# Kernel tuning notes

Measured on AMD Instinct MI355X. Metric: run time of the kernel, lower is better.

Reference implementation:

```python
import jax, jax.numpy as jnp
import numpy as np

N = 50000   # nodes
E = 200000  # edges
G = 2048    # graphs in batch
H = 300     # hidden_dim
L = 5       # nlayer
AF, AV = 9, 128   # atom features, vocab per feature
BF, BV = 3, 16    # bond features, vocab per feature


def setup_inputs() -> dict:
    key = jax.random.key(0)
    ks = jax.random.split(key, 10)
    s = 0.05
    batch = jnp.sort(jax.random.randint(ks[0], (N,), 0, G))
    x = jax.random.randint(ks[1], (N, AF), 0, AV)
    edge_index = jax.random.randint(ks[2], (2, E), 0, N)
    edge_attr = jax.random.randint(ks[3], (E, BF), 0, BV)
    atom_emb = jax.random.normal(ks[4], (AF * AV, H), dtype=jnp.float32) * s
    bond_emb = jax.random.normal(ks[5], (BF * BV, H), dtype=jnp.float32) * s
    W1 = jax.random.normal(ks[6], (L, H, 2 * H), dtype=jnp.float32) * s
    b1 = jnp.zeros((L, 2 * H), jnp.float32)
    g1 = jnp.ones((L, 2 * H), jnp.float32)
    be1 = jnp.zeros((L, 2 * H), jnp.float32)
    W2 = jax.random.normal(ks[7], (L, 2 * H, H), dtype=jnp.float32) * s
    b2 = jnp.zeros((L, H), jnp.float32)
    g2 = jnp.ones((L, H), jnp.float32)   # outer BatchNorm gamma
    be2 = jnp.zeros((L, H), jnp.float32)  # outer BatchNorm beta
    return dict(batch=batch, x=x, edge_index=edge_index, edge_attr=edge_attr,
                atom_emb=atom_emb, bond_emb=bond_emb,
                W1=W1, b1=b1, g1=g1, be1=be1, W2=W2, b2=b2, g2=g2, be2=be2)


def _bn(z, g, b):
    # training-mode BatchNorm1d over the node/batch dim
    m = z.mean(0)
    v = z.var(0)
    return (z - m) * jax.lax.rsqrt(v + 1e-5) * g + b


def reference(batch, x, edge_index, edge_attr, atom_emb, bond_emb,
              W1, b1, g1, be1, W2, b2, g2, be2):
    # AtomEncoder / BondEncoder: sum of per-feature embeddings (flat-table gather)
    h = atom_emb[x + jnp.arange(AF) * AV].sum(axis=1)          # [N, H]
    e = bond_emb[edge_attr + jnp.arange(BF) * BV].sum(axis=1)  # [E, H]
    src, dst = edge_index[0], edge_index[1]
    for i in range(L):
        # GINEConv: out = MLP((1+eps)*x + sum_j relu(x_j + e_ij)), eps=0
        msg = jax.nn.relu(h[src] + e)                          # [E, H]
        agg = jax.ops.segment_sum(msg, dst, num_segments=N)    # [N, H]
        z = h + agg
        z = jax.nn.relu(_bn(z @ W1[i] + b1[i], g1[i], be1[i])) # Linear+BN+ReLU
        z = z @ W2[i] + b2[i]                                  # Linear
        z = _bn(z, g2[i], be2[i])                              # outer BatchNorm
        h = z if i == L - 1 else jax.nn.relu(z)                # dropout p=0.0 -> identity
    xpool = jax.ops.segment_sum(h, batch, num_segments=G)     # global_add_pool
    return (h, xpool)
```

## Files before the change

### kernel.cpp

```cpp
#include <hip/hip_runtime.h>

#define N_NODES 50000
#define N_EDGES 200000
#define N_GRAPHS 2048
#define HDIM 300
#define HDIM2 600
#define NLAYER 5
#define K1P 320
#define N1P 640
#define N2P 384

#define MT1 ((N_NODES + 127) / 128)
#define NWG1 (5 * MT1)
#define NWG2 (3 * MT1)

#define SCAN_BLK 1024
#define NSCAN ((N_NODES + SCAN_BLK - 1) / SCAN_BLK)

typedef __attribute__((ext_vector_type(8))) _Float16 f16x8;
typedef __attribute__((ext_vector_type(8))) unsigned short ushort8;
typedef __attribute__((ext_vector_type(4))) float f32x4;

__device__ __forceinline__ unsigned short f2h(float f) {
    _Float16 h = (_Float16)f;
    return __builtin_bit_cast(unsigned short, h);
}
__device__ __forceinline__ float h2f(unsigned short u) {
    _Float16 h = __builtin_bit_cast(_Float16, u);
    return (float)h;
}

__device__ __forceinline__ int lower_bound_i(const int* a, int n, int key) {
    int lo = 0, hi = n;
    while (lo < hi) { int mid = (lo + hi) >> 1; if (a[mid] < key) lo = mid + 1; else hi = mid; }
    return lo;
}

__device__ __forceinline__ int xcd_swz(int orig, int nwg) {
    int q = nwg >> 3, r = nwg & 7;
    int xcd = orig & 7;
    int base = (xcd < r) ? xcd * (q + 1) : r * (q + 1) + (xcd - r) * q;
    return base + (orig >> 3);
}

__global__ void k_init(int* deg, int* fill, float* s1, float* q1, float* s2, float* q2) {
    int i = blockIdx.x * blockDim.x + threadIdx.x;
    if (i < N_NODES) { deg[i] = 0; fill[i] = 0; }
    if (i < N1P)     { s1[i] = 0.f; q1[i] = 0.f; }
    if (i < K1P)     { s2[i] = 0.f; q2[i] = 0.f; }
}

__global__ void k_atom(const int* __restrict__ x, const float* __restrict__ atom_emb,
                       unsigned short* __restrict__ hf) {
    int idx = blockIdx.x * blockDim.x + threadIdx.x;
    if (idx >= N_NODES * K1P) return;
    int n = idx / K1P;
    int c = idx - n * K1P;
    if (c >= HDIM) { hf[idx] = 0; return; }
    const int* xr = x + n * 9;
    float acc = 0.f;
#pragma unroll
    for (int f = 0; f < 9; ++f) {
        int row = xr[f] + f * 128;
        acc += atom_emb[(size_t)row * HDIM + c];
    }
    hf[idx] = f2h(acc);
}

__global__ void k_deg(const int* __restrict__ dst, int* deg) {
    int j = blockIdx.x * blockDim.x + threadIdx.x;
    if (j < N_EDGES) atomicAdd(&deg[dst[j]], 1);
}

__global__ void k_scan1(const int* __restrict__ deg, int* __restrict__ part,
                        int* __restrict__ psum) {
    __shared__ int buf[SCAN_BLK];
    int b = blockIdx.x, tid = threadIdx.x;
    int i = b * SCAN_BLK + tid;
    int v = (i < N_NODES) ? deg[i] : 0;
    buf[tid] = v;
    __syncthreads();
    for (int off = 1; off < SCAN_BLK; off <<= 1) {
        int t = (tid >= off) ? buf[tid - off] : 0;
        __syncthreads();
        buf[tid] += t;
        __syncthreads();
    }
    if (i < N_NODES) part[i] = buf[tid];
    if (tid == SCAN_BLK - 1) psum[b] = buf[tid];
}

__global__ void k_scan2(int* __restrict__ psum) {
    __shared__ int buf[64];
    int tid = threadIdx.x;
    int v = (tid < NSCAN) ? psum[tid] : 0;
    buf[tid] = v;
    __syncthreads();
    for (int off = 1; off < 64; off <<= 1) {
        int t = (tid >= off) ? buf[tid - off] : 0;
        __syncthreads();
        buf[tid] += t;
        __syncthreads();
    }
    if (tid < NSCAN) psum[tid] = buf[tid] - v;
}

__global__ void k_scan3(const int* __restrict__ part, const int* __restrict__ psum,
                        int* __restrict__ rowptr) {
    int i = blockIdx.x * blockDim.x + threadIdx.x;
    if (i == 0) rowptr[0] = 0;
    if (i < N_NODES) rowptr[i + 1] = part[i] + psum[i / SCAN_BLK];
}

__global__ void k_fill(const int* __restrict__ src, const int* __restrict__ dst,
                       const int* __restrict__ eattr, const int* __restrict__ rowptr,
                       int* fill, int* __restrict__ csr_src, int* __restrict__ csr_att) {
    int j = blockIdx.x * blockDim.x + threadIdx.x;
    if (j < N_EDGES) {
        int d = dst[j];
        int p = atomicAdd(&fill[d], 1);
        int pos = rowptr[d] + p;
        csr_src[pos] = src[j];
        csr_att[pos] = eattr[j * 3 + 0] | (eattr[j * 3 + 1] << 8) | (eattr[j * 3 + 2] << 16);
    }
}

__global__ void k_wconv(const float* __restrict__ W, unsigned short* __restrict__ Bt,
                        int K, int NC, int KPAD, int NPAD) {
    int idx = blockIdx.x * blockDim.x + threadIdx.x;
    int tot = NLAYER * NPAD * KPAD;
    if (idx >= tot) return;
    int l = idx / (NPAD * KPAD);
    int rem = idx - l * NPAD * KPAD;
    int n = rem / KPAD;
    int k = rem - n * KPAD;
    float v = (k < K && n < NC) ? W[((size_t)l * K + k) * NC + n] : 0.f;
    Bt[idx] = f2h(v);
}

template <bool BN>
__global__ __launch_bounds__(128) void k_msg(const unsigned short* __restrict__ hsrc,
                                             const float* __restrict__ sc,
                                             const float* __restrict__ sh,
                                             const int* __restrict__ rowptr,
                                             const int* __restrict__ csr_src,
                                             const int* __restrict__ csr_att,
                                             const float* __restrict__ bond_emb,
                                             unsigned short* __restrict__ zin) {
    int n = blockIdx.x;
    int t = threadIdx.x;
    int cols[3] = { t, t + 128, t + 256 };
    float scv[3] = {0.f, 0.f, 0.f}, shv[3] = {0.f, 0.f, 0.f};
    float acc[3] = {0.f, 0.f, 0.f};
#pragma unroll
    for (int q = 0; q < 3; ++q) {
        int c = cols[q];
        if (c < HDIM) {
            if (BN) { scv[q] = sc[c]; shv[q] = sh[c]; }
            float v = h2f(hsrc[(size_t)n * K1P + c]);
            if (BN) v = fmaxf(v * scv[q] + shv[q], 0.f);
            acc[q] = v;
        }
    }

    int beg = rowptr[n], end = rowptr[n + 1];
    int p = beg;
    for (; p + 2 <= end; p += 2) {
        int s0 = csr_src[p],     a0 = csr_att[p];
        int s1 = csr_src[p + 1], a1 = csr_att[p + 1];
        const unsigned short* h0 = hsrc + (size_t)s0 * K1P;
        const unsigned short* h1 = hsrc + (size_t)s1 * K1P;
        const float* e00 = bond_emb + (size_t)(a0 & 0xff) * HDIM;
        const float* e01 = bond_emb + (size_t)(16 + ((a0 >> 8) & 0xff)) * HDIM;
        const float* e02 = bond_emb + (size_t)(32 + ((a0 >> 16) & 0xff)) * HDIM;
        const float* e10 = bond_emb + (size_t)(a1 & 0xff) * HDIM;
        const float* e11 = bond_emb + (size_t)(16 + ((a1 >> 8) & 0xff)) * HDIM;
        const float* e12 = bond_emb + (size_t)(32 + ((a1 >> 16) & 0xff)) * HDIM;
#pragma unroll
        for (int q = 0; q < 3; ++q) {
            int c = cols[q];
            if (c < HDIM) {
                float v0 = h2f(h0[c]);
                float v1 = h2f(h1[c]);
                if (BN) {
                    v0 = fmaxf(v0 * scv[q] + shv[q], 0.f);
                    v1 = fmaxf(v1 * scv[q] + shv[q], 0.f);
                }
                float m0 = v0 + e00[c] + e01[c] + e02[c];
                float m1 = v1 + e10[c] + e11[c] + e12[c];
                acc[q] += fmaxf(m0, 0.f) + fmaxf(m1, 0.f);
            }
        }
    }
    if (p < end) {
        int s0 = csr_src[p], a0 = csr_att[p];
        const unsigned short* h0 = hsrc + (size_t)s0 * K1P;
        const float* e00 = bond_emb + (size_t)(a0 & 0xff) * HDIM;
        const float* e01 = bond_emb + (size_t)(16 + ((a0 >> 8) & 0xff)) * HDIM;
        const float* e02 = bond_emb + (size_t)(32 + ((a0 >> 16) & 0xff)) * HDIM;
#pragma unroll
        for (int q = 0; q < 3; ++q) {
            int c = cols[q];
            if (c < HDIM) {
                float v0 = h2f(h0[c]);
                if (BN) v0 = fmaxf(v0 * scv[q] + shv[q], 0.f);
                float m0 = v0 + e00[c] + e01[c] + e02[c];
                acc[q] += fmaxf(m0, 0.f);
            }
        }
    }
    unsigned short* zr = zin + (size_t)n * K1P;
#pragma unroll
    for (int q = 0; q < 3; ++q) {
        int c = cols[q];
        if (c < HDIM) zr[c] = f2h(acc[q]);
        else if (c < K1P) zr[c] = 0;
    }
}

__global__ __launch_bounds__(256) void k_mfma1(const unsigned short* __restrict__ A,
                                               const unsigned short* __restrict__ Bt,
                                               const float* __restrict__ bias,
                                               unsigned short* __restrict__ Ch,
                                               float* __restrict__ gsum,
                                               float* __restrict__ gssq) {
    __shared__ unsigned short tA[2][128 * 32];
    __shared__ unsigned short tB[2][128 * 32];
    __shared__ float csum[128], cssq[128];

    const int tid = threadIdx.x;
    const int lane = tid & 63, wid = tid >> 6;
    const int wm = wid >> 1, wn = wid & 1;
    const int wgid = xcd_swz(blockIdx.x, NWG1);
    const int n0 = (wgid % 5) * 128, m0 = (wgid / 5) * 128;
    const int fr = lane & 15, fq = lane >> 4;

    f32x4 acc[4][4] = {};
    const int arow = lane >> 2;
    const int achk = (lane & 3) * 8;
    constexpr int NT = K1P / 32;

    auto stage = [&](int buf, int kt) {
        const int k0 = kt * 32;
#pragma unroll
        for (int i = 0; i < 2; ++i) {
            int grp = i * 4 + wid;
            int grow = m0 + grp * 16 + arow;
            if (grow >= N_NODES) grow = N_NODES - 1;
            const unsigned short* ga = A + (size_t)grow * K1P + k0 + achk;
            __builtin_amdgcn_global_load_lds((const __attribute__((address_space(1))) void*)ga,
                                             (__attribute__((address_space(3))) void*)&tA[buf][grp * 512],
                                             16, 0, 0);
            int gn = n0 + grp * 16 + arow;
            const unsigned short* gb = Bt + (size_t)gn * K1P + k0 + achk;
            __builtin_amdgcn_global_load_lds((const __attribute__((address_space(1))) void*)gb,
                                             (__attribute__((address_space(3))) void*)&tB[buf][grp * 512],
                                             16, 0, 0);
        }
    };

    stage(0, 0);
    __syncthreads();

    int cur = 0;
    for (int kt = 0; kt < NT; ++kt) {
        if (kt + 1 < NT) stage(cur ^ 1, kt + 1);

        f16x8 af[4], bfr[4];
#pragma unroll
        for (int t = 0; t < 4; ++t) {
            af[t]  = *(const f16x8*)&tA[cur][(wm * 64 + t * 16 + fr) * 32 + fq * 8];
            bfr[t] = *(const f16x8*)&tB[cur][(wn * 64 + t * 16 + fr) * 32 + fq * 8];
        }
#pragma unroll
        for (int mt = 0; mt < 4; ++mt)
#pragma unroll
            for (int nt = 0; nt < 4; ++nt)
                acc[mt][nt] = __builtin_amdgcn_mfma_f32_16x16x32_f16(af[mt], bfr[nt], acc[mt][nt], 0, 0, 0);

        __syncthreads();
        cur ^= 1;
    }

    float bv[4];
#pragma unroll
    for (int nt = 0; nt < 4; ++nt) {
        int col = n0 + wn * 64 + nt * 16 + fr;
        bv[nt] = (col < HDIM2) ? bias[col] : 0.f;
    }
    if (tid < 128) { csum[tid] = 0.f; cssq[tid] = 0.f; }
    __syncthreads();

    float colS[4] = {0.f, 0.f, 0.f, 0.f};
    float colQ[4] = {0.f, 0.f, 0.f, 0.f};
#pragma unroll
    for (int mt = 0; mt < 4; ++mt) {
#pragma unroll
        for (int r = 0; r < 4; ++r) {
            int row = m0 + wm * 64 + mt * 16 + fq * 4 + r;
            bool rok = row < N_NODES;
#pragma unroll
            for (int nt = 0; nt < 4; ++nt) {
                int col = n0 + wn * 64 + nt * 16 + fr;
                float v = acc[mt][nt][r] + bv[nt];
                if (rok && col < HDIM2) {
                    Ch[(size_t)row * N1P + col] = f2h(v);
                    colS[nt] += v;
                    colQ[nt] += v * v;
                } else if (rok) {
                    Ch[(size_t)row * N1P + col] = 0;
                }
            }
        }
    }
#pragma unroll
    for (int nt = 0; nt < 4; ++nt) {
        int c = wn * 64 + nt * 16 + fr;
        atomicAdd(&csum[c], colS[nt]);
        atomicAdd(&cssq[c], colQ[nt]);
    }
    __syncthreads();
    if (tid < 128) {
        int col = n0 + tid;
        if (col < HDIM2) {
            atomicAdd(&gsum[col], csum[tid]);
            atomicAdd(&gssq[col], cssq[tid]);
        }
    }
}

__global__ __launch_bounds__(256) void k_mfma2(const unsigned short* __restrict__ z1,
                                               const unsigned short* __restrict__ Bt,
                                               const float* __restrict__ bias,
                                               const unsigned short* __restrict__ scaleAh,
                                               const unsigned short* __restrict__ shiftAh,
                                               unsigned short* __restrict__ Ch,
                                               float* __restrict__ gsum,
                                               float* __restrict__ gssq) {
    __shared__ unsigned short tA[2][128 * 32];
    __shared__ unsigned short tB[2][128 * 32];
    __shared__ float csum[128], cssq[128];

    const int tid = threadIdx.x;
    const int lane = tid & 63, wid = tid >> 6;
    const int wm = wid >> 1, wn = wid & 1;
    const int wgid = xcd_swz(blockIdx.x, NWG2);
    const int n0 = (wgid % 3) * 128, m0 = (wgid / 3) * 128;
    const int fr = lane & 15, fq = lane >> 4;

    f32x4 acc[4][4] = {};
    const int arow = lane >> 2;
    const int achk = (lane & 3) * 8;
    constexpr int NT = N1P / 32;

    auto stage = [&](int buf, int kt) {
        const int k0 = kt * 32;
#pragma unroll
        for (int i = 0; i < 2; ++i) {
            int grp = i * 4 + wid;
            int grow = m0 + grp * 16 + arow;
            if (grow >= N_NODES) grow = N_NODES - 1;
            const unsigned short* ga = z1 + (size_t)grow * N1P + k0 + achk;
            __builtin_amdgcn_global_load_lds((const __attribute__((address_space(1))) void*)ga,
                                             (__attribute__((address_space(3))) void*)&tA[buf][grp * 512],
                                             16, 0, 0);
            int gn = n0 + grp * 16 + arow;
            const unsigned short* gb = Bt + (size_t)gn * N1P + k0 + achk;
            __builtin_amdgcn_global_load_lds((const __attribute__((address_space(1))) void*)gb,
                                             (__attribute__((address_space(3))) void*)&tB[buf][grp * 512],
                                             16, 0, 0);
        }
    };

    stage(0, 0);
    __syncthreads();

    int cur = 0;
    for (int kt = 0; kt < NT; ++kt) {
        if (kt + 1 < NT) stage(cur ^ 1, kt + 1);

        const int kc = kt * 32 + fq * 8;
        f16x8 sa = *(const f16x8*)&scaleAh[kc];
        f16x8 sb = *(const f16x8*)&shiftAh[kc];
        f16x8 af[4], bfr[4];
#pragma unroll
        for (int t = 0; t < 4; ++t) {
            f16x8 z = *(const f16x8*)&tA[cur][(wm * 64 + t * 16 + fr) * 32 + fq * 8];
            f16x8 r;
#pragma unroll
            for (int j = 0; j < 8; ++j) {
                _Float16 v = z[j] * sa[j] + sb[j];
                r[j] = (v > (_Float16)0) ? v : (_Float16)0;
            }
            af[t] = r;
            bfr[t] = *(const f16x8*)&tB[cur][(wn * 64 + t * 16 + fr) * 32 + fq * 8];
        }
#pragma unroll
        for (int mt = 0; mt < 4; ++mt)
#pragma unroll
            for (int nt = 0; nt < 4; ++nt)
                acc[mt][nt] = __builtin_amdgcn_mfma_f32_16x16x32_f16(af[mt], bfr[nt], acc[mt][nt], 0, 0, 0);

        __syncthreads();
        cur ^= 1;
    }

    float bv[4];
#pragma unroll
    for (int nt = 0; nt < 4; ++nt) {
        int col = n0 + wn * 64 + nt * 16 + fr;
        bv[nt] = (col < HDIM) ? bias[col] : 0.f;
    }
    if (tid < 128) { csum[tid] = 0.f; cssq[tid] = 0.f; }
    __syncthreads();

    float colS[4] = {0.f, 0.f, 0.f, 0.f};
    float colQ[4] = {0.f, 0.f, 0.f, 0.f};
#pragma unroll
    for (int mt = 0; mt < 4; ++mt) {
#pragma unroll
        for (int r = 0; r < 4; ++r) {
            int row = m0 + wm * 64 + mt * 16 + fq * 4 + r;
            bool rok = row < N_NODES;
#pragma unroll
            for (int nt = 0; nt < 4; ++nt) {
                int col = n0 + wn * 64 + nt * 16 + fr;
                float v = acc[mt][nt][r] + bv[nt];
                if (rok && col < HDIM) {
                    Ch[(size_t)row * K1P + col] = f2h(v);
                    colS[nt] += v;
                    colQ[nt] += v * v;
                } else if (rok && col < K1P) {
                    Ch[(size_t)row * K1P + col] = 0;
                }
            }
        }
    }
#pragma unroll
    for (int nt = 0; nt < 4; ++nt) {
        int c = wn * 64 + nt * 16 + fr;
        atomicAdd(&csum[c], colS[nt]);
        atomicAdd(&cssq[c], colQ[nt]);
    }
    __syncthreads();
    if (tid < 128) {
        int col = n0 + tid;
        if (col < HDIM) {
            atomicAdd(&gsum[col], csum[tid]);
            atomicAdd(&gssq[col], cssq[tid]);
        }
    }
}

__global__ void k_fin(const float* __restrict__ gsum, const float* __restrict__ gssq,
                      const float* __restrict__ gamma, const float* __restrict__ beta,
                      int C, int CPAD, float* __restrict__ scale, float* __restrict__ shift,
                      unsigned short* scaleh, unsigned short* shifth,
                      float* zs, float* zq, int CZ) {
    int i = blockIdx.x * blockDim.x + threadIdx.x;
    if (i < CPAD) {
        float sc = 0.f, sh = 0.f;
        if (i < C) {
            float m = gsum[i] * (1.f / (float)N_NODES);
            float v = gssq[i] * (1.f / (float)N_NODES) - m * m;
            float rs = rsqrtf(v + 1e-5f);
            sc = rs * gamma[i];
            sh = beta[i] - m * sc;
        }
        scale[i] = sc;
        shift[i] = sh;
        if (scaleh) { scaleh[i] = f2h(sc); shifth[i] = f2h(sh); }
    }
    if (i < CZ) { zs[i] = 0.f; zq[i] = 0.f; }
}

__global__ void k_normf(const unsigned short* __restrict__ z2,
                        const float* __restrict__ scale, const float* __restrict__ shift,
                        float* __restrict__ out_h) {
    int idx = blockIdx.x * blockDim.x + threadIdx.x;
    if (idx >= N_NODES * (K1P / 4)) return;
    int row = idx / (K1P / 4);
    int c = (idx % (K1P / 4)) * 4;
    if (c >= HDIM) return;
    const unsigned short* zr = z2 + (size_t)row * K1P + c;
    float4 o;
    o.x = h2f(zr[0]) * scale[c + 0] + shift[c + 0];
    o.y = h2f(zr[1]) * scale[c + 1] + shift[c + 1];
    o.z = h2f(zr[2]) * scale[c + 2] + shift[c + 2];
    o.w = h2f(zr[3]) * scale[c + 3] + shift[c + 3];
    *(float4*)(out_h + (size_t)row * HDIM + c) = o;
}

__global__ __launch_bounds__(128) void k_pool(const float* __restrict__ hfin,
                                              const int* __restrict__ batch,
                                              float* __restrict__ xpool) {
    int g = blockIdx.x;
    int t = threadIdx.x;
    int start = lower_bound_i(batch, N_NODES, g);
    int end   = lower_bound_i(batch, N_NODES, g + 1);
    int cols[3] = { t, t + 128, t + 256 };
    float acc[3] = {0.f, 0.f, 0.f};
    for (int n = start; n < end; ++n) {
        const float* hr = hfin + (size_t)n * HDIM;
#pragma unroll
        for (int q = 0; q < 3; ++q)
            if (cols[q] < HDIM) acc[q] += hr[cols[q]];
    }
#pragma unroll
    for (int q = 0; q < 3; ++q)
        if (cols[q] < HDIM) xpool[(size_t)g * HDIM + cols[q]] = acc[q];
}

extern "C" void kernel_launch(void* const* d_in, const int* in_sizes, int n_in,
                              void* d_out, int out_size, void* d_ws, size_t ws_size,
                              hipStream_t stream) {
    const int*   batch    = (const int*)d_in[0];
    const int*   x        = (const int*)d_in[1];
    const int*   eidx     = (const int*)d_in[2];
    const int*   eattr    = (const int*)d_in[3];
    const float* atom_emb = (const float*)d_in[4];
    const float* bond_emb = (const float*)d_in[5];
    const float* W1 = (const float*)d_in[6];
    const float* b1 = (const float*)d_in[7];
    const float* g1 = (const float*)d_in[8];
    const float* be1 = (const float*)d_in[9];
    const float* W2 = (const float*)d_in[10];
    const float* b2 = (const float*)d_in[11];
    const float* g2 = (const float*)d_in[12];
    const float* be2 = (const float*)d_in[13];

    const int* src = eidx;
    const int* dst = eidx + N_EDGES;

    float* out_h    = (float*)d_out;
    float* out_pool = (float*)d_out + (size_t)N_NODES * HDIM;

    char* ws = (char*)d_ws;
    size_t off = 0;
    auto alloc = [&](size_t bytes) -> void* {
        void* p = ws + off;
        off += (bytes + 255) & ~(size_t)255;
        return p;
    };
    unsigned short* hf   = (unsigned short*)alloc((size_t)N_NODES * K1P * 2);
    unsigned short* zin  = (unsigned short*)alloc((size_t)N_NODES * K1P * 2);
    unsigned short* z1   = (unsigned short*)alloc((size_t)N_NODES * N1P * 2);
    unsigned short* z2   = (unsigned short*)alloc((size_t)N_NODES * K1P * 2);
    unsigned short* W1t  = (unsigned short*)alloc((size_t)NLAYER * N1P * K1P * 2);
    unsigned short* W2t  = (unsigned short*)alloc((size_t)NLAYER * N2P * N1P * 2);
    int* rowptr  = (int*)alloc((N_NODES + 1) * sizeof(int));
    int* deg     = (int*)alloc(N_NODES * sizeof(int));
    int* fill    = (int*)alloc(N_NODES * sizeof(int));
    int* part    = (int*)alloc(N_NODES * sizeof(int));
    int* psum    = (int*)alloc(64 * sizeof(int));
    int* csr_src = (int*)alloc(N_EDGES * sizeof(int));
    int* csr_att = (int*)alloc(N_EDGES * sizeof(int));
    float* s1     = (float*)alloc(N1P * sizeof(float));
    float* q1     = (float*)alloc(N1P * sizeof(float));
    float* scale1 = (float*)alloc(N1P * sizeof(float));
    float* shift1 = (float*)alloc(N1P * sizeof(float));
    unsigned short* scale1h = (unsigned short*)alloc(N1P * sizeof(short));
    unsigned short* shift1h = (unsigned short*)alloc(N1P * sizeof(short));
    float* s2     = (float*)alloc(K1P * sizeof(float));
    float* q2     = (float*)alloc(K1P * sizeof(float));
    float* scale2 = (float*)alloc(K1P * sizeof(float));
    float* shift2 = (float*)alloc(K1P * sizeof(float));

    k_init<<<(N_NODES + 255) / 256, 256, 0, stream>>>(deg, fill, s1, q1, s2, q2);
    k_atom<<<(N_NODES * K1P + 255) / 256, 256, 0, stream>>>(x, atom_emb, hf);
    k_deg<<<(N_EDGES + 255) / 256, 256, 0, stream>>>(dst, deg);
    k_scan1<<<NSCAN, SCAN_BLK, 0, stream>>>(deg, part, psum);
    k_scan2<<<1, 64, 0, stream>>>(psum);
    k_scan3<<<(N_NODES + 255) / 256, 256, 0, stream>>>(part, psum, rowptr);
    k_fill<<<(N_EDGES + 255) / 256, 256, 0, stream>>>(src, dst, eattr, rowptr,
                                                      fill, csr_src, csr_att);
    {
        int tot1 = NLAYER * N1P * K1P;
        k_wconv<<<(tot1 + 255) / 256, 256, 0, stream>>>(W1, W1t, HDIM, HDIM2, K1P, N1P);
        int tot2 = NLAYER * N2P * N1P;
        k_wconv<<<(tot2 + 255) / 256, 256, 0, stream>>>(W2, W2t, HDIM2, HDIM, N1P, N2P);
    }

    for (int l = 0; l < NLAYER; ++l) {
        if (l == 0) {
            k_msg<false><<<N_NODES, 128, 0, stream>>>(hf, nullptr, nullptr,
                                                      rowptr, csr_src, csr_att, bond_emb, zin);
        } else {
            k_msg<true><<<N_NODES, 128, 0, stream>>>(z2, scale2, shift2,
                                                     rowptr, csr_src, csr_att, bond_emb, zin);
        }

        k_mfma1<<<NWG1, 256, 0, stream>>>(
            zin, W1t + (size_t)l * N1P * K1P, b1 + (size_t)l * HDIM2, z1, s1, q1);

        k_fin<<<3, 256, 0, stream>>>(s1, q1, g1 + (size_t)l * HDIM2, be1 + (size_t)l * HDIM2,
                                     HDIM2, N1P, scale1, shift1, scale1h, shift1h,
                                     s2, q2, K1P);

        k_mfma2<<<NWG2, 256, 0, stream>>>(
            z1, W2t + (size_t)l * N2P * N1P, b2 + (size_t)l * HDIM,
            scale1h, shift1h, z2, s2, q2);

        k_fin<<<3, 256, 0, stream>>>(s2, q2, g2 + (size_t)l * HDIM, be2 + (size_t)l * HDIM,
                                     HDIM, K1P, scale2, shift2, nullptr, nullptr,
                                     s1, q1, N1P);
    }

    k_normf<<<(N_NODES * (K1P / 4) + 255) / 256, 256, 0, stream>>>(
        z2, scale2, shift2, out_h);

    k_pool<<<N_GRAPHS, 128, 0, stream>>>(out_h, batch, out_pool);
}
```

Before: 1.221 ms.

## Map one wavefront per node in message kernel and double GEMM K-step

The message-aggregation kernel now assigns one 64-lane wavefront per node (four nodes per 256-thread block) with five columns per lane, replacing one 128-thread block per node where many threads idled on the 300-wide row. Both MFMA GEMM kernels now stage 64-wide K tiles (two 32-wide halves) per pipeline step, halving the number of barriers and staging rounds. The larger tiles double the LDS footprint per block, which may reduce occupancy.

```diff
diff --git a/kernel.cpp b/kernel.cpp
--- a/kernel.cpp
+++ b/kernel.cpp
@@ -139,7 +139,7 @@
 }
 
 template <bool BN>
-__global__ __launch_bounds__(128) void k_msg(const unsigned short* __restrict__ hsrc,
+__global__ __launch_bounds__(256) void k_msg(const unsigned short* __restrict__ hsrc,
                                              const float* __restrict__ sc,
                                              const float* __restrict__ sh,
                                              const int* __restrict__ rowptr,
@@ -147,14 +147,15 @@
                                              const int* __restrict__ csr_att,
                                              const float* __restrict__ bond_emb,
                                              unsigned short* __restrict__ zin) {
-    int n = blockIdx.x;
-    int t = threadIdx.x;
-    int cols[3] = { t, t + 128, t + 256 };
-    float scv[3] = {0.f, 0.f, 0.f}, shv[3] = {0.f, 0.f, 0.f};
-    float acc[3] = {0.f, 0.f, 0.f};
-#pragma unroll
-    for (int q = 0; q < 3; ++q) {
-        int c = cols[q];
+    int wid = threadIdx.x >> 6, lane = threadIdx.x & 63;
+    int n = blockIdx.x * 4 + wid;
+    if (n >= N_NODES) return;
+
+    float scv[5], shv[5], acc[5];
+#pragma unroll
+    for (int q = 0; q < 5; ++q) {
+        int c = lane + 64 * q;
+        scv[q] = 0.f; shv[q] = 0.f; acc[q] = 0.f;
         if (c < HDIM) {
             if (BN) { scv[q] = sc[c]; shv[q] = sh[c]; }
             float v = h2f(hsrc[(size_t)n * K1P + c]);
@@ -177,8 +178,8 @@
         const float* e11 = bond_emb + (size_t)(16 + ((a1 >> 8) & 0xff)) * HDIM;
         const float* e12 = bond_emb + (size_t)(32 + ((a1 >> 16) & 0xff)) * HDIM;
 #pragma unroll
-        for (int q = 0; q < 3; ++q) {
-            int c = cols[q];
+        for (int q = 0; q < 5; ++q) {
+            int c = lane + 64 * q;
             if (c < HDIM) {
                 float v0 = h2f(h0[c]);
                 float v1 = h2f(h1[c]);
@@ -199,8 +200,8 @@
         const float* e01 = bond_emb + (size_t)(16 + ((a0 >> 8) & 0xff)) * HDIM;
         const float* e02 = bond_emb + (size_t)(32 + ((a0 >> 16) & 0xff)) * HDIM;
 #pragma unroll
-        for (int q = 0; q < 3; ++q) {
-            int c = cols[q];
+        for (int q = 0; q < 5; ++q) {
+            int c = lane + 64 * q;
             if (c < HDIM) {
                 float v0 = h2f(h0[c]);
                 if (BN) v0 = fmaxf(v0 * scv[q] + shv[q], 0.f);
@@ -211,10 +212,9 @@
     }
     unsigned short* zr = zin + (size_t)n * K1P;
 #pragma unroll
-    for (int q = 0; q < 3; ++q) {
-        int c = cols[q];
-        if (c < HDIM) zr[c] = f2h(acc[q]);
-        else if (c < K1P) zr[c] = 0;
+    for (int q = 0; q < 5; ++q) {
+        int c = lane + 64 * q;
+        zr[c] = (c < HDIM) ? f2h(acc[q]) : 0;
     }
 }
 
@@ -224,8 +224,8 @@
                                                unsigned short* __restrict__ Ch,
                                                float* __restrict__ gsum,
                                                float* __restrict__ gssq) {
-    __shared__ unsigned short tA[2][128 * 32];
-    __shared__ unsigned short tB[2][128 * 32];
+    __shared__ unsigned short tA[2][8192];
+    __shared__ unsigned short tB[2][8192];
     __shared__ float csum[128], cssq[128];
 
     const int tid = threadIdx.x;
@@ -238,24 +238,27 @@
     f32x4 acc[4][4] = {};
     const int arow = lane >> 2;
     const int achk = (lane & 3) * 8;
-    constexpr int NT = K1P / 32;
-
-    auto stage = [&](int buf, int kt) {
-        const int k0 = kt * 32;
-#pragma unroll
-        for (int i = 0; i < 2; ++i) {
-            int grp = i * 4 + wid;
-            int grow = m0 + grp * 16 + arow;
-            if (grow >= N_NODES) grow = N_NODES - 1;
-            const unsigned short* ga = A + (size_t)grow * K1P + k0 + achk;
-            __builtin_amdgcn_global_load_lds((const __attribute__((address_space(1))) void*)ga,
-                                             (__attribute__((address_space(3))) void*)&tA[buf][grp * 512],
-                                             16, 0, 0);
-            int gn = n0 + grp * 16 + arow;
-            const unsigned short* gb = Bt + (size_t)gn * K1P + k0 + achk;
-            __builtin_amdgcn_global_load_lds((const __attribute__((address_space(1))) void*)gb,
-                                             (__attribute__((address_space(3))) void*)&tB[buf][grp * 512],
-                                             16, 0, 0);
+    constexpr int NT2 = K1P / 64;
+
+    auto stage = [&](int buf, int kt2) {
+        const int k0 = kt2 * 64;
+#pragma unroll
+        for (int hh = 0; hh < 2; ++hh) {
+#pragma unroll
+            for (int i = 0; i < 2; ++i) {
+                int grp = i * 4 + wid;
+                int grow = m0 + grp * 16 + arow;
+                if (grow >= N_NODES) grow = N_NODES - 1;
+                const unsigned short* ga = A + (size_t)grow * K1P + k0 + hh * 32 + achk;
+                __builtin_amdgcn_global_load_lds((const __attribute__((address_space(1))) void*)ga,
+                                                 (__attribute__((address_space(3))) void*)&tA[buf][hh * 4096 + grp * 512],
+                                                 16, 0, 0);
+                int gn = n0 + grp * 16 + arow;
+                const unsigned short* gb = Bt + (size_t)gn * K1P + k0 + hh * 32 + achk;
+                __builtin_amdgcn_global_load_lds((const __attribute__((address_space(1))) void*)gb,
+                                                 (__attribute__((address_space(3))) void*)&tB[buf][hh * 4096 + grp * 512],
+                                                 16, 0, 0);
+            }
         }
     };
 
@@ -263,20 +266,23 @@
     __syncthreads();
 
     int cur = 0;
-    for (int kt = 0; kt < NT; ++kt) {
-        if (kt + 1 < NT) stage(cur ^ 1, kt + 1);
-
-        f16x8 af[4], bfr[4];
-#pragma unroll
-        for (int t = 0; t < 4; ++t) {
-            af[t]  = *(const f16x8*)&tA[cur][(wm * 64 + t * 16 + fr) * 32 + fq * 8];
-            bfr[t] = *(const f16x8*)&tB[cur][(wn * 64 + t * 16 + fr) * 32 + fq * 8];
-        }
-#pragma unroll
-        for (int mt = 0; mt < 4; ++mt)
-#pragma unroll
-            for (int nt = 0; nt < 4; ++nt)
-                acc[mt][nt] = __builtin_amdgcn_mfma_f32_16x16x32_f16(af[mt], bfr[nt], acc[mt][nt], 0, 0, 0);
+    for (int kt2 = 0; kt2 < NT2; ++kt2) {
+        if (kt2 + 1 < NT2) stage(cur ^ 1, kt2 + 1);
+
+#pragma unroll
+        for (int hh = 0; hh < 2; ++hh) {
+            f16x8 af[4], bfr[4];
+#pragma unroll
+            for (int t = 0; t < 4; ++t) {
+                af[t]  = *(const f16x8*)&tA[cur][hh * 4096 + (wm * 64 + t * 16 + fr) * 32 + fq * 8];
+                bfr[t] = *(const f16x8*)&tB[cur][hh * 4096 + (wn * 64 + t * 16 + fr) * 32 + fq * 8];
+            }
+#pragma unroll
+            for (int mt = 0; mt < 4; ++mt)
+#pragma unroll
+                for (int nt = 0; nt < 4; ++nt)
+                    acc[mt][nt] = __builtin_amdgcn_mfma_f32_16x16x32_f16(af[mt], bfr[nt], acc[mt][nt], 0, 0, 0);
+        }
 
         __syncthreads();
         cur ^= 1;
@@ -337,8 +343,8 @@
                                                unsigned short* __restrict__ Ch,
                                                float* __restrict__ gsum,
                                                float* __restrict__ gssq) {
-    __shared__ unsigned short tA[2][128 * 32];
-    __shared__ unsigned short tB[2][128 * 32];
+    __shared__ unsigned short tA[2][8192];
+    __shared__ unsigned short tB[2][8192];
     __shared__ float csum[128], cssq[128];
 
     const int tid = threadIdx.x;
@@ -351,24 +357,27 @@
     f32x4 acc[4][4] = {};
     const int arow = lane >> 2;
     const int achk = (lane & 3) * 8;
-    constexpr int NT = N1P / 32;
-
-    auto stage = [&](int buf, int kt) {
-        const int k0 = kt * 32;
-#pragma unroll
-        for (int i = 0; i < 2; ++i) {
-            int grp = i * 4 + wid;
-            int grow = m0 + grp * 16 + arow;
-            if (grow >= N_NODES) grow = N_NODES - 1;
-            const unsigned short* ga = z1 + (size_t)grow * N1P + k0 + achk;
-            __builtin_amdgcn_global_load_lds((const __attribute__((address_space(1))) void*)ga,
-                                             (__attribute__((address_space(3))) void*)&tA[buf][grp * 512],
-                                             16, 0, 0);
-            int gn = n0 + grp * 16 + arow;
-            const unsigned short* gb = Bt + (size_t)gn * N1P + k0 + achk;
-            __builtin_amdgcn_global_load_lds((const __attribute__((address_space(1))) void*)gb,
-                                             (__attribute__((address_space(3))) void*)&tB[buf][grp * 512],
-                                             16, 0, 0);
+    constexpr int NT2 = N1P / 64;
+
+    auto stage = [&](int buf, int kt2) {
+        const int k0 = kt2 * 64;
+#pragma unroll
+        for (int hh = 0; hh < 2; ++hh) {
+#pragma unroll
+            for (int i = 0; i < 2; ++i) {
+                int grp = i * 4 + wid;
+                int grow = m0 + grp * 16 + arow;
+                if (grow >= N_NODES) grow = N_NODES - 1;
+                const unsigned short* ga = z1 + (size_t)grow * N1P + k0 + hh * 32 + achk;
+                __builtin_amdgcn_global_load_lds((const __attribute__((address_space(1))) void*)ga,
+                                                 (__attribute__((address_space(3))) void*)&tA[buf][hh * 4096 + grp * 512],
+                                                 16, 0, 0);
+                int gn = n0 + grp * 16 + arow;
+                const unsigned short* gb = Bt + (size_t)gn * N1P + k0 + hh * 32 + achk;
+                __builtin_amdgcn_global_load_lds((const __attribute__((address_space(1))) void*)gb,
+                                                 (__attribute__((address_space(3))) void*)&tB[buf][hh * 4096 + grp * 512],
+                                                 16, 0, 0);
+            }
         }
     };
 
@@ -376,30 +385,33 @@
     __syncthreads();
 
     int cur = 0;
-    for (int kt = 0; kt < NT; ++kt) {
-        if (kt + 1 < NT) stage(cur ^ 1, kt + 1);
-
-        const int kc = kt * 32 + fq * 8;
-        f16x8 sa = *(const f16x8*)&scaleAh[kc];
-        f16x8 sb = *(const f16x8*)&shiftAh[kc];
-        f16x8 af[4], bfr[4];
-#pragma unroll
-        for (int t = 0; t < 4; ++t) {
-            f16x8 z = *(const f16x8*)&tA[cur][(wm * 64 + t * 16 + fr) * 32 + fq * 8];
-            f16x8 r;
-#pragma unroll
-            for (int j = 0; j < 8; ++j) {
-                _Float16 v = z[j] * sa[j] + sb[j];
-                r[j] = (v > (_Float16)0) ? v : (_Float16)0;
-            }
-            af[t] = r;
-            bfr[t] = *(const f16x8*)&tB[cur][(wn * 64 + t * 16 + fr) * 32 + fq * 8];
-        }
-#pragma unroll
-        for (int mt = 0; mt < 4; ++mt)
-#pragma unroll
-            for (int nt = 0; nt < 4; ++nt)
-                acc[mt][nt] = __builtin_amdgcn_mfma_f32_16x16x32_f16(af[mt], bfr[nt], acc[mt][nt], 0, 0, 0);
+    for (int kt2 = 0; kt2 < NT2; ++kt2) {
+        if (kt2 + 1 < NT2) stage(cur ^ 1, kt2 + 1);
+
+#pragma unroll
+        for (int hh = 0; hh < 2; ++hh) {
+            const int kc = kt2 * 64 + hh * 32 + fq * 8;
+            f16x8 sa = *(const f16x8*)&scaleAh[kc];
+            f16x8 sb = *(const f16x8*)&shiftAh[kc];
+            f16x8 af[4], bfr[4];
+#pragma unroll
+            for (int t = 0; t < 4; ++t) {
+                f16x8 z = *(const f16x8*)&tA[cur][hh * 4096 + (wm * 64 + t * 16 + fr) * 32 + fq * 8];
+                f16x8 r;
+#pragma unroll
+                for (int j = 0; j < 8; ++j) {
+                    _Float16 v = z[j] * sa[j] + sb[j];
+                    r[j] = (v > (_Float16)0) ? v : (_Float16)0;
+                }
+                af[t] = r;
+                bfr[t] = *(const f16x8*)&tB[cur][hh * 4096 + (wn * 64 + t * 16 + fr) * 32 + fq * 8];
+            }
+#pragma unroll
+            for (int mt = 0; mt < 4; ++mt)
+#pragma unroll
+                for (int nt = 0; nt < 4; ++nt)
+                    acc[mt][nt] = __builtin_amdgcn_mfma_f32_16x16x32_f16(af[mt], bfr[nt], acc[mt][nt], 0, 0, 0);
+        }
 
         __syncthreads();
         cur ^= 1;
@@ -581,13 +593,14 @@
         k_wconv<<<(tot2 + 255) / 256, 256, 0, stream>>>(W2, W2t, HDIM2, HDIM, N1P, N2P);
     }
 
+    int msg_grid = (N_NODES + 3) / 4;
     for (int l = 0; l < NLAYER; ++l) {
         if (l == 0) {
-            k_msg<false><<<N_NODES, 128, 0, stream>>>(hf, nullptr, nullptr,
+            k_msg<false><<<msg_grid, 256, 0, stream>>>(hf, nullptr, nullptr,
+                                                       rowptr, csr_src, csr_att, bond_emb, zin);
+        } else {
+            k_msg<true><<<msg_grid, 256, 0, stream>>>(z2, scale2, shift2,
                                                       rowptr, csr_src, csr_att, bond_emb, zin);
-        } else {
-            k_msg<true><<<N_NODES, 128, 0, stream>>>(z2, scale2, shift2,
-                                                     rowptr, csr_src, csr_att, bond_emb, zin);
         }
 
         k_mfma1<<<NWG1, 256, 0, stream>>>(
```

Result: slower. 1.308 ms (+7.2%).

## Map one wavefront per node in message kernel and add occupancy hints to GEMMs

Applied to the files above, without the earlier changes.

The message/aggregation kernel changes from one 128-thread block per node (3 columns per thread, with idle lanes in the last pass) to one 64-lane wavefront per node, four nodes per 256-thread block, each lane covering 5 columns. This cuts the block count by four and removes cross-wave work for a single node, which lowers launch and scheduling overhead and avoids partially idle waves. The two MFMA GEMM kernels also get min-blocks-per-CU launch bounds (4 and 3), which limit register use to raise occupancy but may cause spills.

```diff
diff --git a/kernel.cpp b/kernel.cpp
--- a/kernel.cpp
+++ b/kernel.cpp
@@ -139,7 +139,7 @@
 }
 
 template <bool BN>
-__global__ __launch_bounds__(128) void k_msg(const unsigned short* __restrict__ hsrc,
+__global__ __launch_bounds__(256) void k_msg(const unsigned short* __restrict__ hsrc,
                                              const float* __restrict__ sc,
                                              const float* __restrict__ sh,
                                              const int* __restrict__ rowptr,
@@ -147,14 +147,15 @@
                                              const int* __restrict__ csr_att,
                                              const float* __restrict__ bond_emb,
                                              unsigned short* __restrict__ zin) {
-    int n = blockIdx.x;
-    int t = threadIdx.x;
-    int cols[3] = { t, t + 128, t + 256 };
-    float scv[3] = {0.f, 0.f, 0.f}, shv[3] = {0.f, 0.f, 0.f};
-    float acc[3] = {0.f, 0.f, 0.f};
-#pragma unroll
-    for (int q = 0; q < 3; ++q) {
-        int c = cols[q];
+    int wid = threadIdx.x >> 6, lane = threadIdx.x & 63;
+    int n = blockIdx.x * 4 + wid;
+    if (n >= N_NODES) return;
+
+    float scv[5], shv[5], acc[5];
+#pragma unroll
+    for (int q = 0; q < 5; ++q) {
+        int c = lane + 64 * q;
+        scv[q] = 0.f; shv[q] = 0.f; acc[q] = 0.f;
         if (c < HDIM) {
             if (BN) { scv[q] = sc[c]; shv[q] = sh[c]; }
             float v = h2f(hsrc[(size_t)n * K1P + c]);
@@ -177,8 +178,8 @@
         const float* e11 = bond_emb + (size_t)(16 + ((a1 >> 8) & 0xff)) * HDIM;
         const float* e12 = bond_emb + (size_t)(32 + ((a1 >> 16) & 0xff)) * HDIM;
 #pragma unroll
-        for (int q = 0; q < 3; ++q) {
-            int c = cols[q];
+        for (int q = 0; q < 5; ++q) {
+            int c = lane + 64 * q;
             if (c < HDIM) {
                 float v0 = h2f(h0[c]);
                 float v1 = h2f(h1[c]);
@@ -199,8 +200,8 @@
         const float* e01 = bond_emb + (size_t)(16 + ((a0 >> 8) & 0xff)) * HDIM;
         const float* e02 = bond_emb + (size_t)(32 + ((a0 >> 16) & 0xff)) * HDIM;
 #pragma unroll
-        for (int q = 0; q < 3; ++q) {
-            int c = cols[q];
+        for (int q = 0; q < 5; ++q) {
+            int c = lane + 64 * q;
             if (c < HDIM) {
                 float v0 = h2f(h0[c]);
                 if (BN) v0 = fmaxf(v0 * scv[q] + shv[q], 0.f);
@@ -211,19 +212,18 @@
     }
     unsigned short* zr = zin + (size_t)n * K1P;
 #pragma unroll
-    for (int q = 0; q < 3; ++q) {
-        int c = cols[q];
-        if (c < HDIM) zr[c] = f2h(acc[q]);
-        else if (c < K1P) zr[c] = 0;
-    }
-}
-
-__global__ __launch_bounds__(256) void k_mfma1(const unsigned short* __restrict__ A,
-                                               const unsigned short* __restrict__ Bt,
-                                               const float* __restrict__ bias,
-                                               unsigned short* __restrict__ Ch,
-                                               float* __restrict__ gsum,
-                                               float* __restrict__ gssq) {
+    for (int q = 0; q < 5; ++q) {
+        int c = lane + 64 * q;
+        zr[c] = (c < HDIM) ? f2h(acc[q]) : 0;
+    }
+}
+
+__global__ __launch_bounds__(256, 4) void k_mfma1(const unsigned short* __restrict__ A,
+                                                  const unsigned short* __restrict__ Bt,
+                                                  const float* __restrict__ bias,
+                                                  unsigned short* __restrict__ Ch,
+                                                  float* __restrict__ gsum,
+                                                  float* __restrict__ gssq) {
     __shared__ unsigned short tA[2][128 * 32];
     __shared__ unsigned short tB[2][128 * 32];
     __shared__ float csum[128], cssq[128];
@@ -329,14 +329,14 @@
     }
 }
 
-__global__ __launch_bounds__(256) void k_mfma2(const unsigned short* __restrict__ z1,
-                                               const unsigned short* __restrict__ Bt,
-                                               const float* __restrict__ bias,
-                                               const unsigned short* __restrict__ scaleAh,
-                                               const unsigned short* __restrict__ shiftAh,
-                                               unsigned short* __restrict__ Ch,
-                                               float* __restrict__ gsum,
-                                               float* __restrict__ gssq) {
+__global__ __launch_bounds__(256, 3) void k_mfma2(const unsigned short* __restrict__ z1,
+                                                  const unsigned short* __restrict__ Bt,
+                                                  const float* __restrict__ bias,
+                                                  const unsigned short* __restrict__ scaleAh,
+                                                  const unsigned short* __restrict__ shiftAh,
+                                                  unsigned short* __restrict__ Ch,
+                                                  float* __restrict__ gsum,
+                                                  float* __restrict__ gssq) {
     __shared__ unsigned short tA[2][128 * 32];
     __shared__ unsigned short tB[2][128 * 32];
     __shared__ float csum[128], cssq[128];
@@ -581,13 +581,14 @@
         k_wconv<<<(tot2 + 255) / 256, 256, 0, stream>>>(W2, W2t, HDIM2, HDIM, N1P, N2P);
     }
 
+    int msg_grid = (N_NODES + 3) / 4;
     for (int l = 0; l < NLAYER; ++l) {
         if (l == 0) {
-            k_msg<false><<<N_NODES, 128, 0, stream>>>(hf, nullptr, nullptr,
+            k_msg<false><<<msg_grid, 256, 0, stream>>>(hf, nullptr, nullptr,
+                                                       rowptr, csr_src, csr_att, bond_emb, zin);
+        } else {
+            k_msg<true><<<msg_grid, 256, 0, stream>>>(z2, scale2, shift2,
                                                       rowptr, csr_src, csr_att, bond_emb, zin);
-        } else {
-            k_msg<true><<<N_NODES, 128, 0, stream>>>(z2, scale2, shift2,
-                                                     rowptr, csr_src, csr_att, bond_emb, zin);
         }
 
         k_mfma1<<<NWG1, 256, 0, stream>>>(
```

Result: faster. 1.193 ms (-2.2%).
